# Optimization experiments

Hardware: AMD Instinct MI355X
Metric: run time of the kernel (lower is better)

## Reference

```python
import jax, jax.numpy as jnp
import numpy as np

EPS = 1e-7
PI = np.pi


def _vel_to_R(vel):
    # vel: [..., 3] -> rotation matrix [..., 3, 3] (ZY convention from spherical angles)
    rho = jnp.linalg.norm(vel, axis=-1, keepdims=True)
    theta = jnp.arctan2(vel[..., 1:2], vel[..., 0:1])
    theta = theta + (theta < 0).astype(theta.dtype) * (2.0 * PI)  # symmetric_theta=False
    phi = jnp.arccos(jnp.clip(vel[..., 2:3] / (rho + EPS), -1.0, 1.0))
    ct, st = jnp.cos(theta)[..., 0], jnp.sin(theta)[..., 0]
    cp, sp = jnp.cos(phi)[..., 0], jnp.sin(phi)[..., 0]
    z = jnp.zeros_like(ct)
    R = jnp.stack([
        jnp.stack([cp * ct, -st, sp * ct], -1),
        jnp.stack([cp * st, ct, sp * st], -1),
        jnp.stack([-sp, z, cp], -1),
    ], -2)
    return R


def _rotate(R, x):
    return jnp.einsum('...ij,...j->...i', R, x)


def setup_inputs() -> dict:
    key = jax.random.key(0)
    B, N, H, D = 128, 100, 128, 3
    in_size = 2 * D  # 6
    nef = 3 * D + D * (D - 1) // 2 + in_size  # 18 edge features
    ks = jax.random.split(key, 12)

    inputs = jax.random.normal(ks[0], (B, N, in_size), jnp.float32)

    # fully connected edges (no self loops)
    send_np, recv_np = np.nonzero(~np.eye(N, dtype=bool))
    send_edges = jnp.asarray(send_np, jnp.int32)
    recv_edges = jnp.asarray(recv_np, jnp.int32)

    def lin(k, fin, fout):
        return jax.random.normal(k, (fin, fout), jnp.float32) / np.sqrt(fin)

    return dict(
        inputs=inputs,
        W1=lin(ks[1], nef, H), b1=jnp.zeros((H,), jnp.float32),
        W2=lin(ks[2], H, H), b2=jnp.zeros((H,), jnp.float32),
        Wr=lin(ks[3], in_size, H), br=jnp.zeros((H,), jnp.float32),
        W3=lin(ks[4], H, H), b3=jnp.zeros((H,), jnp.float32),
        W4=lin(ks[5], H, H), b4=jnp.zeros((H,), jnp.float32),
        W5=lin(ks[6], H, in_size), b5=jnp.zeros((in_size,), jnp.float32),
        send_edges=send_edges, recv_edges=recv_edges,
    )


def reference(inputs, W1, b1, W2, b2, Wr, br, W3, b3, W4, b4, W5, b5,
              send_edges, recv_edges):
    D = 3
    B, N, _ = inputs.shape

    # ---- Localizer.canonicalize_inputs ----
    vel = inputs[..., D:2 * D]
    Rnode = _vel_to_R(vel)                       # [B,N,3,3]
    Rinv_node = jnp.swapaxes(Rnode, -1, -2)
    canon_vel = _rotate(Rinv_node, vel)
    rel_feat = jnp.concatenate([jnp.zeros_like(canon_vel), canon_vel], -1)  # [B,N,6]

    # ---- Localizer.create_edge_attr ----
    x_j = inputs[:, send_edges]                  # [B,E,6] senders
    x_i = inputs[:, recv_edges]                  # [B,E,6] receivers
    R = _vel_to_R(x_i[..., D:2 * D])
    R_inv = jnp.swapaxes(R, -1, -2)
    rel_pos = x_j[..., :D] - x_i[..., :D]
    rot_rel = _rotate(R_inv, rel_pos)
    send_R = _vel_to_R(x_j[..., D:2 * D])
    rot_or = R_inv @ send_R
    euler = jnp.stack([
        jnp.arctan2(rot_or[..., 1, 0], rot_or[..., 0, 0]),
        jnp.arcsin(-rot_or[..., 2, 0]),
        jnp.arctan2(rot_or[..., 2, 1], rot_or[..., 2, 2]),
    ], -1) / PI
    dist = jnp.linalg.norm(rel_pos, axis=-1, keepdims=True)
    rho_e = jnp.linalg.norm(rot_rel, axis=-1, keepdims=True)
    theta_e = jnp.arctan2(rot_rel[..., 1:2], rot_rel[..., 0:1])  # symmetric theta
    phi_e = jnp.arccos(jnp.clip(rot_rel[..., 2:3] / (rho_e + EPS), -1.0, 1.0))
    rot_vel = _rotate(R_inv, x_j[..., D:2 * D])
    edge_attr = jnp.concatenate(
        [rot_rel, euler, dist, theta_e, phi_e, rot_vel], -1)   # [B,E,12]
    edge_attr = jnp.concatenate([edge_attr, rel_feat[:, recv_edges]], -1)  # [B,E,18]

    # ---- GNN: edge MLP + scatter-mean + out MLP (dropout off in eval) ----
    h = jax.nn.silu(edge_attr @ W1 + b1) @ W2 + b2               # [B,E,H]
    agg = jnp.zeros((B, N, h.shape[-1]), h.dtype).at[:, recv_edges].add(h)
    cnt = jnp.zeros((N,), h.dtype).at[recv_edges].add(1.0)
    agg = agg / jnp.maximum(cnt, 1.0)[None, :, None]             # scatter mean
    aug = agg + rel_feat @ Wr + br
    p = jax.nn.relu(aug @ W3 + b3)
    p = jax.nn.relu(p @ W4 + b4)
    pred = p @ W5 + b5                                           # [B,N,6]

    # ---- Globalizer: rotate each 3-vector chunk back to global frame ----
    gl = jnp.concatenate(
        [_rotate(Rnode, pred[..., i:i + D]) for i in range(0, pred.shape[-1], D)], -1)
    return inputs + gl
```

## Files before the change

### kernel.cpp

```cpp
#include <hip/hip_runtime.h>
#include <math.h>

#define EPSF 1e-7f
constexpr int NN  = 100;
constexpr int DEG = 99;
constexpr int IN  = 6;
constexpr int H   = 128;
constexpr int G   = 4;
constexpr float INV_PI = 0.3183098861837907f;
constexpr float LOG2E  = 1.4426950408889634f;
constexpr float LN2    = 0.6931471805599453f;

typedef __attribute__((ext_vector_type(4))) _Float16 half4;
typedef __attribute__((ext_vector_type(8))) _Float16 half8;
typedef __attribute__((ext_vector_type(4))) float f32x4;

constexpr int XST = 144;
constexpr int SXS = 15;
constexpr int TS  = 50;
constexpr int NT  = 25;

__device__ __forceinline__ float clampf(float x, float lo, float hi) {
    return fminf(fmaxf(x, lo), hi);
}
__device__ __forceinline__ float sig2(float y) {
    return __builtin_amdgcn_rcpf(1.f + __builtin_amdgcn_exp2f(-y));
}
__device__ __forceinline__ float fast_atan2(float y, float x) {
    float ax = fabsf(x), ay = fabsf(y);
    float mx = fmaxf(ax, ay), mn = fminf(ax, ay);
    float r = mn * __builtin_amdgcn_rcpf(fmaxf(mx, 1e-35f));
    float r2 = r * r;
    float p = fmaf(r2, -0.0851330f, 0.1801410f);
    p = fmaf(r2, p, -0.3302995f);
    p = fmaf(r2, p, 0.9998660f);
    float t = r * p;
    t = (ay > ax) ? (1.5707963267948966f - t) : t;
    t = (x < 0.f) ? (3.14159265358979323f - t) : t;
    return copysignf(t, y);
}
__device__ __forceinline__ float fast_asin(float z) {
    return fast_atan2(z, sqrtf(fmaxf(0.f, (1.f - z) * (1.f + z))));
}
__device__ __forceinline__ float fast_acos(float z) {
    return fast_atan2(sqrtf(fmaxf(0.f, (1.f - z) * (1.f + z))), z);
}
__device__ __forceinline__ void vel_to_R(float vx, float vy, float vz, float* R) {
    float rho = sqrtf(vx * vx + vy * vy + vz * vz);
    float rxy = sqrtf(vx * vx + vy * vy);
    float inv = __builtin_amdgcn_rcpf(rxy);
    bool big = rxy > 1e-30f;
    float ct = big ? vx * inv : 1.f;
    float st = big ? vy * inv : 0.f;
    float cp = clampf(vz * __builtin_amdgcn_rcpf(rho + EPSF), -1.f, 1.f);
    float sp = sqrtf(fmaxf(0.f, 1.f - cp * cp));
    R[0] = cp * ct; R[1] = -st; R[2] = sp * ct;
    R[3] = cp * st; R[4] = ct;  R[5] = sp * st;
    R[6] = -sp;     R[7] = 0.f; R[8] = cp;
}

__global__ void conv_w(const float* __restrict__ W1, const float* __restrict__ W2,
                       const float* __restrict__ W3, const float* __restrict__ W4,
                       half4* __restrict__ w1f, half8* __restrict__ wmlp) {
    int t = blockIdx.x * blockDim.x + threadIdx.x;
    if (t >= 104 * 64) return;
    int L = t & 63, f = t >> 6;
    int m = L & 15, qd = L >> 4;
    if (f < 8) {
        int n = f * 16 + m;
        half4 v;
#pragma unroll
        for (int j = 0; j < 4; ++j) {
            int k = qd * 4 + j;
            v[j] = (k < 12) ? (_Float16)(W1[k * H + n] * LOG2E) : (_Float16)0.f;
        }
        w1f[f * 64 + L] = v;
    } else {
        int ff = f - 8;
        int layer = ff >> 5, rest = ff & 31;
        int kt = rest >> 3, nt = rest & 7;
        const float* W = (layer == 0) ? W2 : (layer == 1) ? W3 : W4;
        float scale = (layer == 0) ? LN2 : 1.f;
        int n = nt * 16 + m;
        half8 v;
#pragma unroll
        for (int j = 0; j < 8; ++j)
            v[j] = (_Float16)(W[(kt * 32 + qd * 8 + j) * H + n] * scale);
        wmlp[((layer * 4 + kt) * 8 + nt) * 64 + L] = v;
    }
}

__global__ __launch_bounds__(256, 8)
void locs_fused(const float* __restrict__ in,
                const float* __restrict__ W1, const float* __restrict__ b1,
                const float* __restrict__ b2,
                const float* __restrict__ Wr, const float* __restrict__ br,
                const float* __restrict__ b3, const float* __restrict__ b4,
                const float* __restrict__ W5, const float* __restrict__ b5,
                const half4* __restrict__ w1f, const half8* __restrict__ wmlp,
                float* __restrict__ out) {
    __shared__ _Float16 hpool[NT * TS * 4];
    __shared__ float sxr[NN * SXS];
    __shared__ float xFp[G * 132];
    __shared__ float cvF[16];
    __shared__ float pbF[G * 96];
    __shared__ float predF[G * 8];

    const int tid = threadIdx.x;
    const int L   = tid & 63;
    const int wv  = tid >> 6;
    const int q   = L >> 4;
    const int lm  = L & 15;
    const int bn0 = blockIdx.x * G;
    const int bB  = bn0 / NN;
    const int n0  = bn0 - bB * NN;

    {
        half4 z = {0, 0, 0, 0};
        for (int i = tid; i < NT * TS; i += 256) *(half4*)&hpool[i * 4] = z;
    }
    if (tid < NN) {
        const float* xi = in + (bB * NN + tid) * IN;
        float R[9];
        float px = xi[0], py = xi[1], pz = xi[2];
        float vx = xi[3], vy = xi[4], vz = xi[5];
        vel_to_R(vx, vy, vz, R);
        float* dst = sxr + tid * SXS;
#pragma unroll
        for (int k = 0; k < 9; ++k) dst[k] = R[k];
        dst[9] = px; dst[10] = py; dst[11] = pz;
        dst[12] = vx; dst[13] = vy; dst[14] = vz;
        int g = tid - n0;
        if ((unsigned)g < (unsigned)G) {
            cvF[g * 4 + 0] = R[0] * vx + R[3] * vy + R[6] * vz;
            cvF[g * 4 + 1] = R[1] * vx + R[4] * vy + R[7] * vz;
            cvF[g * 4 + 2] = R[2] * vx + R[5] * vy + R[8] * vz;
        }
    }
    __syncthreads();

    float bs[2];
    {
        float cv0 = cvF[q * 4 + 0], cv1 = cvF[q * 4 + 1], cv2 = cvF[q * 4 + 2];
#pragma unroll
        for (int i = 0; i < 2; ++i) {
            int ch = wv * 32 + i * 16 + lm;
            bs[i] = (b1[ch] + cv0 * W1[15 * H + ch] + cv1 * W1[16 * H + ch]
                   + cv2 * W1[17 * H + ch]) * LOG2E;
        }
    }
    half4 bfr[2];
#pragma unroll
    for (int i = 0; i < 2; ++i) bfr[i] = w1f[(wv * 2 + i) * 64 + L];

#pragma unroll
    for (int rnd = 0; rnd < 2; ++rnd) {
        int j = tid + rnd * 256;
        if (j < G * DEG) {
            int g = j / DEG;
            int e = j - g * DEG;
            int nG = n0 + g;
            int s = e < nG ? e : e + 1;
            const float* rn = sxr + nG * SXS;
            const float* rs = sxr + s * SXS;
            float Rn[9];
#pragma unroll
            for (int k = 0; k < 9; ++k) Rn[k] = rn[k];
            float rel0 = rs[9] - rn[9], rel1 = rs[10] - rn[10], rel2 = rs[11] - rn[11];
            float vjx = rs[12], vjy = rs[13], vjz = rs[14];
            float Rs0 = rs[0], Rs1 = rs[1], Rs2 = rs[2];
            float Rs3 = rs[3], Rs4 = rs[4], Rs5 = rs[5];
            float Rs6 = rs[6], Rs7 = rs[7], Rs8 = rs[8];
            float rr0 = Rn[0] * rel0 + Rn[3] * rel1 + Rn[6] * rel2;
            float rr1 = Rn[1] * rel0 + Rn[4] * rel1 + Rn[7] * rel2;
            float rr2 = Rn[2] * rel0 + Rn[5] * rel1 + Rn[8] * rel2;
            float ro00 = Rn[0] * Rs0 + Rn[3] * Rs3 + Rn[6] * Rs6;
            float ro10 = Rn[1] * Rs0 + Rn[4] * Rs3 + Rn[7] * Rs6;
            float ro20 = Rn[2] * Rs0 + Rn[5] * Rs3 + Rn[8] * Rs6;
            float ro21 = Rn[2] * Rs1 + Rn[5] * Rs4 + Rn[8] * Rs7;
            float ro22 = Rn[2] * Rs2 + Rn[5] * Rs5 + Rn[8] * Rs8;
            float dist = sqrtf(rel0 * rel0 + rel1 * rel1 + rel2 * rel2);
            half4 f0, f1, f2;
            f0[0] = (_Float16)rr0; f0[1] = (_Float16)rr1; f0[2] = (_Float16)rr2;
            f0[3] = (_Float16)(fast_atan2(ro10, ro00) * INV_PI);
            f1[0] = (_Float16)(fast_asin(clampf(-ro20, -1.f, 1.f)) * INV_PI);
            f1[1] = (_Float16)(fast_atan2(ro21, ro22) * INV_PI);
            f1[2] = (_Float16)dist;
            f1[3] = (_Float16)fast_atan2(rr1, rr0);
            f2[0] = (_Float16)fast_acos(clampf(rr2 * __builtin_amdgcn_rcpf(dist + EPSF), -1.f, 1.f));
            f2[1] = (_Float16)(Rn[0] * vjx + Rn[3] * vjy + Rn[6] * vjz);
            f2[2] = (_Float16)(Rn[1] * vjx + Rn[4] * vjy + Rn[7] * vjz);
            f2[3] = (_Float16)(Rn[2] * vjx + Rn[5] * vjy + Rn[8] * vjz);
            int t = e >> 2;
            int mrow = g * 4 + (e & 3);
            _Float16* dst = hpool + (t * TS + mrow) * 4;
            *(half4*)(dst +   0)      = f0;
            *(half4*)(dst + 16 * 4)   = f1;
            *(half4*)(dst + 32 * 4)   = f2;
        }
    }
    __syncthreads();

    {
        float part[2] = {0.f, 0.f};
        f32x4 c[2];
#pragma unroll
        for (int i = 0; i < 2; ++i) c[i] = (f32x4){bs[i], bs[i], bs[i], bs[i]};
        const int loff = (q < 3) ? (q * 16 + lm) : 48;
        half4 a_cur = *(const half4*)&hpool[(0 * TS + loff) * 4];
#pragma unroll
        for (int t = 0; t < NT; ++t) {
            half4 a_next;
            if (t < NT - 1) a_next = *(const half4*)&hpool[((t + 1) * TS + loff) * 4];
            f32x4 d0 = __builtin_amdgcn_mfma_f32_16x16x16f16(a_cur, bfr[0], c[0], 0, 0, 0);
            f32x4 d1 = __builtin_amdgcn_mfma_f32_16x16x16f16(a_cur, bfr[1], c[1], 0, 0, 0);
#pragma unroll
            for (int r = 0; r < 4; ++r) {
                part[0] += d0[r] * sig2(d0[r]);
                part[1] += d1[r] * sig2(d1[r]);
            }
            a_cur = a_next;
        }
#pragma unroll
        for (int i = 0; i < 2; ++i)
            xFp[q * 132 + wv * 32 + i * 16 + lm] = part[i] - bs[i] * sig2(bs[i]);
    }
    __syncthreads();

    _Float16* xh = hpool;
#pragma unroll
    for (int layer = 0; layer < 3; ++layer) {
        {
            int col = tid & 127, rh = tid >> 7;
#pragma unroll
            for (int r = 0; r < 2; ++r) {
                int row = r * 2 + rh;
                xh[row * XST + col] = (_Float16)xFp[row * 132 + col];
            }
        }
        half8 bh[8];
#pragma unroll
        for (int kt = 0; kt < 4; ++kt) {
            int base = ((layer * 4 + kt) * 8 + wv * 2) * 64 + L;
#pragma unroll
            for (int i = 0; i < 2; ++i) bh[kt * 2 + i] = wmlp[base + i * 64];
        }
        __syncthreads();
        int rowb = (lm & 3) * XST;
        half8 ah[4];
#pragma unroll
        for (int kt = 0; kt < 4; ++kt)
            ah[kt] = *(const half8*)&xh[rowb + kt * 32 + q * 8];
        f32x4 acc[2];
#pragma unroll
        for (int i = 0; i < 2; ++i) acc[i] = (f32x4){0.f, 0.f, 0.f, 0.f};
#pragma unroll
        for (int kt = 0; kt < 4; ++kt)
#pragma unroll
            for (int i = 0; i < 2; ++i)
                acc[i] = __builtin_amdgcn_mfma_f32_16x16x32_f16(ah[kt], bh[kt * 2 + i],
                                                                acc[i], 0, 0, 0);
        __syncthreads();
        if (L < 16) {
#pragma unroll
            for (int i = 0; i < 2; ++i) {
                int ch = (wv * 2 + i) * 16 + lm;
                if (layer == 0) {
                    float b2c = b2[ch], brc = br[ch];
                    float w3c = Wr[3 * H + ch], w4c = Wr[4 * H + ch], w5c = Wr[5 * H + ch];
#pragma unroll
                    for (int r = 0; r < 4; ++r)
                        xFp[r * 132 + ch] = acc[i][r] * (1.f / 99.f) + b2c
                                          + cvF[r * 4 + 0] * w3c + cvF[r * 4 + 1] * w4c
                                          + cvF[r * 4 + 2] * w5c + brc;
                } else {
                    float bb = (layer == 1) ? b3[ch] : b4[ch];
#pragma unroll
                    for (int r = 0; r < 4; ++r)
                        xFp[r * 132 + ch] = fmaxf(0.f, acc[i][r] + bb);
                }
            }
        }
        __syncthreads();
    }

    if (tid < 96) {
        int o = tid >> 4, sl = tid & 15, kb = sl * 8;
        float w5[8];
#pragma unroll
        for (int j = 0; j < 8; ++j) w5[j] = W5[(kb + j) * IN + o];
#pragma unroll
        for (int g = 0; g < G; ++g) {
            float s = 0.f;
#pragma unroll
            for (int j = 0; j < 8; ++j) s = fmaf(xFp[g * 132 + kb + j], w5[j], s);
            pbF[g * 96 + sl * 6 + o] = s;
        }
    }
    __syncthreads();
    if (tid < 24) {
        int g = tid / 6, o = tid - g * 6;
        float s = b5[o];
#pragma unroll
        for (int sl = 0; sl < 16; ++sl) s += pbF[g * 96 + sl * 6 + o];
        predF[g * 8 + o] = s;
    }
    __syncthreads();
    if (tid < 24) {
        int g = tid / 6, o = tid - g * 6;
        int r = (o < 3) ? o : o - 3;
        int off = (o < 3) ? 0 : 3;
        const float* Rg = sxr + (n0 + g) * SXS;
        float gl = Rg[r * 3 + 0] * predF[g * 8 + off + 0]
                 + Rg[r * 3 + 1] * predF[g * 8 + off + 1]
                 + Rg[r * 3 + 2] * predF[g * 8 + off + 2];
        int bng = bn0 + g;
        out[bng * IN + o] = Rg[9 + o] + gl;
    }
}

extern "C" void kernel_launch(void* const* d_in, const int* in_sizes, int n_in,
                              void* d_out, int out_size, void* d_ws, size_t ws_size,
                              hipStream_t stream) {
    const float* in = (const float*)d_in[0];
    const float* W1 = (const float*)d_in[1];
    const float* b1 = (const float*)d_in[2];
    const float* W2 = (const float*)d_in[3];
    const float* b2 = (const float*)d_in[4];
    const float* Wr = (const float*)d_in[5];
    const float* br = (const float*)d_in[6];
    const float* W3 = (const float*)d_in[7];
    const float* b3 = (const float*)d_in[8];
    const float* W4 = (const float*)d_in[9];
    const float* b4 = (const float*)d_in[10];
    const float* W5 = (const float*)d_in[11];
    const float* b5 = (const float*)d_in[12];
    float* out = (float*)d_out;

    half4* w1f  = (half4*)d_ws;
    half8* wmlp = (half8*)((char*)d_ws + 4096);

    const int BN = in_sizes[0] / IN;
    conv_w<<<26, 256, 0, stream>>>(W1, W2, W3, W4, w1f, wmlp);
    locs_fused<<<BN / G, 256, 0, stream>>>(in, W1, b1, b2, Wr, br, b3, b4,
                                           W5, b5, w1f, wmlp, out);
}
```

Measured before the change: 127.3 us.

## Use polynomial SiLU without reciprocal and store MLP activations directly as fp16

Replaces the sigmoid-based SiLU (exp2 plus reciprocal) in the edge aggregation loop with a form that uses exp2 of -|d| and a degree-4 polynomial, removing the rcp transcendental. The fp32 staging buffer for MLP activations is dropped. Each layer now writes fp16 straight into a dedicated shared buffer, which removes the per-layer fp32-to-fp16 conversion pass and one barrier per layer. The cost is polynomial approximation error in SiLU and fp16 rounding of the final-layer activations before W5.

```diff
diff --git a/kernel.cpp b/kernel.cpp
--- a/kernel.cpp
+++ b/kernel.cpp
@@ -20,11 +20,19 @@
 constexpr int TS  = 50;
 constexpr int NT  = 25;
 
+constexpr float PB0 = 0.99974609f;
+constexpr float PB1 = -0.98610892f;
+constexpr float PB2 = 0.87197520f;
+constexpr float PB3 = -0.54230560f;
+constexpr float PB4 = 0.15687296f;
+
 __device__ __forceinline__ float clampf(float x, float lo, float hi) {
     return fminf(fmaxf(x, lo), hi);
 }
-__device__ __forceinline__ float sig2(float y) {
-    return __builtin_amdgcn_rcpf(1.f + __builtin_amdgcn_exp2f(-y));
+__device__ __forceinline__ float silu2(float d) {
+    float u = __builtin_amdgcn_exp2f(-fabsf(d));
+    float p = fmaf(fmaf(fmaf(fmaf(PB4, u, PB3), u, PB2), u, PB1), u, PB0);
+    return fmaf(p, fabsf(d), fminf(d, 0.f));
 }
 __device__ __forceinline__ float fast_atan2(float y, float x) {
     float ax = fabsf(x), ay = fabsf(y);
@@ -101,7 +109,7 @@
                 float* __restrict__ out) {
     __shared__ _Float16 hpool[NT * TS * 4];
     __shared__ float sxr[NN * SXS];
-    __shared__ float xFp[G * 132];
+    __shared__ _Float16 xh[G * XST];
     __shared__ float cvF[16];
     __shared__ float pbF[G * 96];
     __shared__ float predF[G * 8];
@@ -216,28 +224,19 @@
             f32x4 d1 = __builtin_amdgcn_mfma_f32_16x16x16f16(a_cur, bfr[1], c[1], 0, 0, 0);
 #pragma unroll
             for (int r = 0; r < 4; ++r) {
-                part[0] += d0[r] * sig2(d0[r]);
-                part[1] += d1[r] * sig2(d1[r]);
+                part[0] += silu2(d0[r]);
+                part[1] += silu2(d1[r]);
             }
             a_cur = a_next;
         }
 #pragma unroll
         for (int i = 0; i < 2; ++i)
-            xFp[q * 132 + wv * 32 + i * 16 + lm] = part[i] - bs[i] * sig2(bs[i]);
-    }
-    __syncthreads();
-
-    _Float16* xh = hpool;
+            xh[q * XST + wv * 32 + i * 16 + lm] = (_Float16)(part[i] - silu2(bs[i]));
+    }
+    __syncthreads();
+
 #pragma unroll
     for (int layer = 0; layer < 3; ++layer) {
-        {
-            int col = tid & 127, rh = tid >> 7;
-#pragma unroll
-            for (int r = 0; r < 2; ++r) {
-                int row = r * 2 + rh;
-                xh[row * XST + col] = (_Float16)xFp[row * 132 + col];
-            }
-        }
         half8 bh[8];
 #pragma unroll
         for (int kt = 0; kt < 4; ++kt) {
@@ -245,7 +244,6 @@
 #pragma unroll
             for (int i = 0; i < 2; ++i) bh[kt * 2 + i] = wmlp[base + i * 64];
         }
-        __syncthreads();
         int rowb = (lm & 3) * XST;
         half8 ah[4];
 #pragma unroll
@@ -270,14 +268,14 @@
                     float w3c = Wr[3 * H + ch], w4c = Wr[4 * H + ch], w5c = Wr[5 * H + ch];
 #pragma unroll
                     for (int r = 0; r < 4; ++r)
-                        xFp[r * 132 + ch] = acc[i][r] * (1.f / 99.f) + b2c
+                        xh[r * XST + ch] = (_Float16)(acc[i][r] * (1.f / 99.f) + b2c
                                           + cvF[r * 4 + 0] * w3c + cvF[r * 4 + 1] * w4c
-                                          + cvF[r * 4 + 2] * w5c + brc;
+                                          + cvF[r * 4 + 2] * w5c + brc);
                 } else {
                     float bb = (layer == 1) ? b3[ch] : b4[ch];
 #pragma unroll
                     for (int r = 0; r < 4; ++r)
-                        xFp[r * 132 + ch] = fmaxf(0.f, acc[i][r] + bb);
+                        xh[r * XST + ch] = (_Float16)fmaxf(0.f, acc[i][r] + bb);
                 }
             }
         }
@@ -291,9 +289,10 @@
         for (int j = 0; j < 8; ++j) w5[j] = W5[(kb + j) * IN + o];
 #pragma unroll
         for (int g = 0; g < G; ++g) {
+            half8 xv = *(const half8*)&xh[g * XST + kb];
             float s = 0.f;
 #pragma unroll
-            for (int j = 0; j < 8; ++j) s = fmaf(xFp[g * 132 + kb + j], w5[j], s);
+            for (int j = 0; j < 8; ++j) s = fmaf((float)xv[j], w5[j], s);
             pbF[g * 96 + sl * 6 + o] = s;
         }
     }
```

Result: slower. 142.4 us (+11.8%).

## Process two node groups per block to reuse per-batch rotation setup

Applied to the files above, without the earlier changes.

Each block now loops over two consecutive groups of four nodes, halving the grid. The per-batch node rotation table in shared memory is built once and recomputed only when the second group starts a new batch element. This amortizes the vel_to_R prologue and the weight-fragment loads across twice the work. The trade-off is fewer blocks and serialized per-block work, plus extra barriers and re-zeroing of padded rows.

```diff
diff --git a/kernel.cpp b/kernel.cpp
--- a/kernel.cpp
+++ b/kernel.cpp
@@ -111,211 +111,226 @@
     const int wv  = tid >> 6;
     const int q   = L >> 4;
     const int lm  = L & 15;
-    const int bn0 = blockIdx.x * G;
-    const int bB  = bn0 / NN;
-    const int n0  = bn0 - bB * NN;
-
-    {
-        half4 z = {0, 0, 0, 0};
-        for (int i = tid; i < NT * TS; i += 256) *(half4*)&hpool[i * 4] = z;
-    }
-    if (tid < NN) {
-        const float* xi = in + (bB * NN + tid) * IN;
-        float R[9];
-        float px = xi[0], py = xi[1], pz = xi[2];
-        float vx = xi[3], vy = xi[4], vz = xi[5];
-        vel_to_R(vx, vy, vz, R);
-        float* dst = sxr + tid * SXS;
-#pragma unroll
-        for (int k = 0; k < 9; ++k) dst[k] = R[k];
-        dst[9] = px; dst[10] = py; dst[11] = pz;
-        dst[12] = vx; dst[13] = vy; dst[14] = vz;
-        int g = tid - n0;
-        if ((unsigned)g < (unsigned)G) {
-            cvF[g * 4 + 0] = R[0] * vx + R[3] * vy + R[6] * vz;
-            cvF[g * 4 + 1] = R[1] * vx + R[4] * vy + R[7] * vz;
-            cvF[g * 4 + 2] = R[2] * vx + R[5] * vy + R[8] * vz;
-        }
-    }
-    __syncthreads();
-
-    float bs[2];
-    {
-        float cv0 = cvF[q * 4 + 0], cv1 = cvF[q * 4 + 1], cv2 = cvF[q * 4 + 2];
-#pragma unroll
-        for (int i = 0; i < 2; ++i) {
-            int ch = wv * 32 + i * 16 + lm;
-            bs[i] = (b1[ch] + cv0 * W1[15 * H + ch] + cv1 * W1[16 * H + ch]
-                   + cv2 * W1[17 * H + ch]) * LOG2E;
-        }
-    }
+
     half4 bfr[2];
 #pragma unroll
     for (int i = 0; i < 2; ++i) bfr[i] = w1f[(wv * 2 + i) * 64 + L];
 
-#pragma unroll
+#pragma unroll 1
     for (int rnd = 0; rnd < 2; ++rnd) {
-        int j = tid + rnd * 256;
-        if (j < G * DEG) {
-            int g = j / DEG;
-            int e = j - g * DEG;
-            int nG = n0 + g;
-            int s = e < nG ? e : e + 1;
-            const float* rn = sxr + nG * SXS;
-            const float* rs = sxr + s * SXS;
-            float Rn[9];
-#pragma unroll
-            for (int k = 0; k < 9; ++k) Rn[k] = rn[k];
-            float rel0 = rs[9] - rn[9], rel1 = rs[10] - rn[10], rel2 = rs[11] - rn[11];
-            float vjx = rs[12], vjy = rs[13], vjz = rs[14];
-            float Rs0 = rs[0], Rs1 = rs[1], Rs2 = rs[2];
-            float Rs3 = rs[3], Rs4 = rs[4], Rs5 = rs[5];
-            float Rs6 = rs[6], Rs7 = rs[7], Rs8 = rs[8];
-            float rr0 = Rn[0] * rel0 + Rn[3] * rel1 + Rn[6] * rel2;
-            float rr1 = Rn[1] * rel0 + Rn[4] * rel1 + Rn[7] * rel2;
-            float rr2 = Rn[2] * rel0 + Rn[5] * rel1 + Rn[8] * rel2;
-            float ro00 = Rn[0] * Rs0 + Rn[3] * Rs3 + Rn[6] * Rs6;
-            float ro10 = Rn[1] * Rs0 + Rn[4] * Rs3 + Rn[7] * Rs6;
-            float ro20 = Rn[2] * Rs0 + Rn[5] * Rs3 + Rn[8] * Rs6;
-            float ro21 = Rn[2] * Rs1 + Rn[5] * Rs4 + Rn[8] * Rs7;
-            float ro22 = Rn[2] * Rs2 + Rn[5] * Rs5 + Rn[8] * Rs8;
-            float dist = sqrtf(rel0 * rel0 + rel1 * rel1 + rel2 * rel2);
-            half4 f0, f1, f2;
-            f0[0] = (_Float16)rr0; f0[1] = (_Float16)rr1; f0[2] = (_Float16)rr2;
-            f0[3] = (_Float16)(fast_atan2(ro10, ro00) * INV_PI);
-            f1[0] = (_Float16)(fast_asin(clampf(-ro20, -1.f, 1.f)) * INV_PI);
-            f1[1] = (_Float16)(fast_atan2(ro21, ro22) * INV_PI);
-            f1[2] = (_Float16)dist;
-            f1[3] = (_Float16)fast_atan2(rr1, rr0);
-            f2[0] = (_Float16)fast_acos(clampf(rr2 * __builtin_amdgcn_rcpf(dist + EPSF), -1.f, 1.f));
-            f2[1] = (_Float16)(Rn[0] * vjx + Rn[3] * vjy + Rn[6] * vjz);
-            f2[2] = (_Float16)(Rn[1] * vjx + Rn[4] * vjy + Rn[7] * vjz);
-            f2[3] = (_Float16)(Rn[2] * vjx + Rn[5] * vjy + Rn[8] * vjz);
-            int t = e >> 2;
-            int mrow = g * 4 + (e & 3);
-            _Float16* dst = hpool + (t * TS + mrow) * 4;
-            *(half4*)(dst +   0)      = f0;
-            *(half4*)(dst + 16 * 4)   = f1;
-            *(half4*)(dst + 32 * 4)   = f2;
-        }
-    }
-    __syncthreads();
-
-    {
-        float part[2] = {0.f, 0.f};
-        f32x4 c[2];
-#pragma unroll
-        for (int i = 0; i < 2; ++i) c[i] = (f32x4){bs[i], bs[i], bs[i], bs[i]};
-        const int loff = (q < 3) ? (q * 16 + lm) : 48;
-        half4 a_cur = *(const half4*)&hpool[(0 * TS + loff) * 4];
-#pragma unroll
-        for (int t = 0; t < NT; ++t) {
-            half4 a_next;
-            if (t < NT - 1) a_next = *(const half4*)&hpool[((t + 1) * TS + loff) * 4];
-            f32x4 d0 = __builtin_amdgcn_mfma_f32_16x16x16f16(a_cur, bfr[0], c[0], 0, 0, 0);
-            f32x4 d1 = __builtin_amdgcn_mfma_f32_16x16x16f16(a_cur, bfr[1], c[1], 0, 0, 0);
-#pragma unroll
-            for (int r = 0; r < 4; ++r) {
-                part[0] += d0[r] * sig2(d0[r]);
-                part[1] += d1[r] * sig2(d1[r]);
-            }
-            a_cur = a_next;
-        }
-#pragma unroll
-        for (int i = 0; i < 2; ++i)
-            xFp[q * 132 + wv * 32 + i * 16 + lm] = part[i] - bs[i] * sig2(bs[i]);
-    }
-    __syncthreads();
-
-    _Float16* xh = hpool;
-#pragma unroll
-    for (int layer = 0; layer < 3; ++layer) {
+        const int bn0 = (blockIdx.x * 2 + rnd) * G;
+        const int bB  = bn0 / NN;
+        const int n0  = bn0 - bB * NN;
+
+        if (rnd == 0) {
+            half4 z = {0, 0, 0, 0};
+            for (int i = tid; i < NT * TS; i += 256) *(half4*)&hpool[i * 4] = z;
+        }
+        if (rnd == 0 || n0 == 0) {
+            if (tid < NN) {
+                const float* xi = in + (bB * NN + tid) * IN;
+                float R[9];
+                float px = xi[0], py = xi[1], pz = xi[2];
+                float vx = xi[3], vy = xi[4], vz = xi[5];
+                vel_to_R(vx, vy, vz, R);
+                float* dst = sxr + tid * SXS;
+#pragma unroll
+                for (int k = 0; k < 9; ++k) dst[k] = R[k];
+                dst[9] = px; dst[10] = py; dst[11] = pz;
+                dst[12] = vx; dst[13] = vy; dst[14] = vz;
+            }
+        }
+        __syncthreads();
+        if (tid < G) {
+            const float* rg = sxr + (n0 + tid) * SXS;
+            float vx = rg[12], vy = rg[13], vz = rg[14];
+            cvF[tid * 4 + 0] = rg[0] * vx + rg[3] * vy + rg[6] * vz;
+            cvF[tid * 4 + 1] = rg[1] * vx + rg[4] * vy + rg[7] * vz;
+            cvF[tid * 4 + 2] = rg[2] * vx + rg[5] * vy + rg[8] * vz;
+        }
+        __syncthreads();
+
+        float bs[2];
         {
-            int col = tid & 127, rh = tid >> 7;
-#pragma unroll
-            for (int r = 0; r < 2; ++r) {
-                int row = r * 2 + rh;
-                xh[row * XST + col] = (_Float16)xFp[row * 132 + col];
-            }
-        }
-        half8 bh[8];
-#pragma unroll
-        for (int kt = 0; kt < 4; ++kt) {
-            int base = ((layer * 4 + kt) * 8 + wv * 2) * 64 + L;
-#pragma unroll
-            for (int i = 0; i < 2; ++i) bh[kt * 2 + i] = wmlp[base + i * 64];
-        }
-        __syncthreads();
-        int rowb = (lm & 3) * XST;
-        half8 ah[4];
-#pragma unroll
-        for (int kt = 0; kt < 4; ++kt)
-            ah[kt] = *(const half8*)&xh[rowb + kt * 32 + q * 8];
-        f32x4 acc[2];
-#pragma unroll
-        for (int i = 0; i < 2; ++i) acc[i] = (f32x4){0.f, 0.f, 0.f, 0.f};
-#pragma unroll
-        for (int kt = 0; kt < 4; ++kt)
+            float cv0 = cvF[q * 4 + 0], cv1 = cvF[q * 4 + 1], cv2 = cvF[q * 4 + 2];
+#pragma unroll
+            for (int i = 0; i < 2; ++i) {
+                int ch = wv * 32 + i * 16 + lm;
+                bs[i] = (b1[ch] + cv0 * W1[15 * H + ch] + cv1 * W1[16 * H + ch]
+                       + cv2 * W1[17 * H + ch]) * LOG2E;
+            }
+        }
+
+        if (rnd && tid < NT) {
+            half4 z = {0, 0, 0, 0};
+            *(half4*)&hpool[(tid * TS + 48) * 4] = z;
+        }
+
+#pragma unroll
+        for (int rr = 0; rr < 2; ++rr) {
+            int j = tid + rr * 256;
+            if (j < G * DEG) {
+                int g = j / DEG;
+                int e = j - g * DEG;
+                int nG = n0 + g;
+                int s = e < nG ? e : e + 1;
+                const float* rn = sxr + nG * SXS;
+                const float* rs = sxr + s * SXS;
+                float Rn[9];
+#pragma unroll
+                for (int k = 0; k < 9; ++k) Rn[k] = rn[k];
+                float rel0 = rs[9] - rn[9], rel1 = rs[10] - rn[10], rel2 = rs[11] - rn[11];
+                float vjx = rs[12], vjy = rs[13], vjz = rs[14];
+                float Rs0 = rs[0], Rs1 = rs[1], Rs2 = rs[2];
+                float Rs3 = rs[3], Rs4 = rs[4], Rs5 = rs[5];
+                float Rs6 = rs[6], Rs7 = rs[7], Rs8 = rs[8];
+                float rr0 = Rn[0] * rel0 + Rn[3] * rel1 + Rn[6] * rel2;
+                float rr1 = Rn[1] * rel0 + Rn[4] * rel1 + Rn[7] * rel2;
+                float rr2 = Rn[2] * rel0 + Rn[5] * rel1 + Rn[8] * rel2;
+                float ro00 = Rn[0] * Rs0 + Rn[3] * Rs3 + Rn[6] * Rs6;
+                float ro10 = Rn[1] * Rs0 + Rn[4] * Rs3 + Rn[7] * Rs6;
+                float ro20 = Rn[2] * Rs0 + Rn[5] * Rs3 + Rn[8] * Rs6;
+                float ro21 = Rn[2] * Rs1 + Rn[5] * Rs4 + Rn[8] * Rs7;
+                float ro22 = Rn[2] * Rs2 + Rn[5] * Rs5 + Rn[8] * Rs8;
+                float dist = sqrtf(rel0 * rel0 + rel1 * rel1 + rel2 * rel2);
+                half4 f0, f1, f2;
+                f0[0] = (_Float16)rr0; f0[1] = (_Float16)rr1; f0[2] = (_Float16)rr2;
+                f0[3] = (_Float16)(fast_atan2(ro10, ro00) * INV_PI);
+                f1[0] = (_Float16)(fast_asin(clampf(-ro20, -1.f, 1.f)) * INV_PI);
+                f1[1] = (_Float16)(fast_atan2(ro21, ro22) * INV_PI);
+                f1[2] = (_Float16)dist;
+                f1[3] = (_Float16)fast_atan2(rr1, rr0);
+                f2[0] = (_Float16)fast_acos(clampf(rr2 * __builtin_amdgcn_rcpf(dist + EPSF), -1.f, 1.f));
+                f2[1] = (_Float16)(Rn[0] * vjx + Rn[3] * vjy + Rn[6] * vjz);
+                f2[2] = (_Float16)(Rn[1] * vjx + Rn[4] * vjy + Rn[7] * vjz);
+                f2[3] = (_Float16)(Rn[2] * vjx + Rn[5] * vjy + Rn[8] * vjz);
+                int t = e >> 2;
+                int mrow = g * 4 + (e & 3);
+                _Float16* dst = hpool + (t * TS + mrow) * 4;
+                *(half4*)(dst +   0)      = f0;
+                *(half4*)(dst + 16 * 4)   = f1;
+                *(half4*)(dst + 32 * 4)   = f2;
+            }
+        }
+        __syncthreads();
+
+        {
+            float part[2] = {0.f, 0.f};
+            f32x4 c[2];
+#pragma unroll
+            for (int i = 0; i < 2; ++i) c[i] = (f32x4){bs[i], bs[i], bs[i], bs[i]};
+            const int loff = (q < 3) ? (q * 16 + lm) : 48;
+            half4 a_cur = *(const half4*)&hpool[(0 * TS + loff) * 4];
+#pragma unroll
+            for (int t = 0; t < NT; ++t) {
+                half4 a_next;
+                if (t < NT - 1) a_next = *(const half4*)&hpool[((t + 1) * TS + loff) * 4];
+                f32x4 d0 = __builtin_amdgcn_mfma_f32_16x16x16f16(a_cur, bfr[0], c[0], 0, 0, 0);
+                f32x4 d1 = __builtin_amdgcn_mfma_f32_16x16x16f16(a_cur, bfr[1], c[1], 0, 0, 0);
+#pragma unroll
+                for (int r = 0; r < 4; ++r) {
+                    part[0] += d0[r] * sig2(d0[r]);
+                    part[1] += d1[r] * sig2(d1[r]);
+                }
+                a_cur = a_next;
+            }
 #pragma unroll
             for (int i = 0; i < 2; ++i)
-                acc[i] = __builtin_amdgcn_mfma_f32_16x16x32_f16(ah[kt], bh[kt * 2 + i],
-                                                                acc[i], 0, 0, 0);
-        __syncthreads();
-        if (L < 16) {
-#pragma unroll
-            for (int i = 0; i < 2; ++i) {
-                int ch = (wv * 2 + i) * 16 + lm;
-                if (layer == 0) {
-                    float b2c = b2[ch], brc = br[ch];
-                    float w3c = Wr[3 * H + ch], w4c = Wr[4 * H + ch], w5c = Wr[5 * H + ch];
-#pragma unroll
-                    for (int r = 0; r < 4; ++r)
-                        xFp[r * 132 + ch] = acc[i][r] * (1.f / 99.f) + b2c
-                                          + cvF[r * 4 + 0] * w3c + cvF[r * 4 + 1] * w4c
-                                          + cvF[r * 4 + 2] * w5c + brc;
-                } else {
-                    float bb = (layer == 1) ? b3[ch] : b4[ch];
-#pragma unroll
-                    for (int r = 0; r < 4; ++r)
-                        xFp[r * 132 + ch] = fmaxf(0.f, acc[i][r] + bb);
+                xFp[q * 132 + wv * 32 + i * 16 + lm] = part[i] - bs[i] * sig2(bs[i]);
+        }
+        __syncthreads();
+
+        _Float16* xh = hpool;
+#pragma unroll
+        for (int layer = 0; layer < 3; ++layer) {
+            {
+                int col = tid & 127, rh = tid >> 7;
+#pragma unroll
+                for (int r = 0; r < 2; ++r) {
+                    int row = r * 2 + rh;
+                    xh[row * XST + col] = (_Float16)xFp[row * 132 + col];
                 }
             }
-        }
-        __syncthreads();
-    }
-
-    if (tid < 96) {
-        int o = tid >> 4, sl = tid & 15, kb = sl * 8;
-        float w5[8];
-#pragma unroll
-        for (int j = 0; j < 8; ++j) w5[j] = W5[(kb + j) * IN + o];
-#pragma unroll
-        for (int g = 0; g < G; ++g) {
-            float s = 0.f;
-#pragma unroll
-            for (int j = 0; j < 8; ++j) s = fmaf(xFp[g * 132 + kb + j], w5[j], s);
-            pbF[g * 96 + sl * 6 + o] = s;
-        }
-    }
-    __syncthreads();
-    if (tid < 24) {
-        int g = tid / 6, o = tid - g * 6;
-        float s = b5[o];
-#pragma unroll
-        for (int sl = 0; sl < 16; ++sl) s += pbF[g * 96 + sl * 6 + o];
-        predF[g * 8 + o] = s;
-    }
-    __syncthreads();
-    if (tid < 24) {
-        int g = tid / 6, o = tid - g * 6;
-        int r = (o < 3) ? o : o - 3;
-        int off = (o < 3) ? 0 : 3;
-        const float* Rg = sxr + (n0 + g) * SXS;
-        float gl = Rg[r * 3 + 0] * predF[g * 8 + off + 0]
-                 + Rg[r * 3 + 1] * predF[g * 8 + off + 1]
-                 + Rg[r * 3 + 2] * predF[g * 8 + off + 2];
-        int bng = bn0 + g;
-        out[bng * IN + o] = Rg[9 + o] + gl;
+            half8 bh[8];
+#pragma unroll
+            for (int kt = 0; kt < 4; ++kt) {
+                int base = ((layer * 4 + kt) * 8 + wv * 2) * 64 + L;
+#pragma unroll
+                for (int i = 0; i < 2; ++i) bh[kt * 2 + i] = wmlp[base + i * 64];
+            }
+            __syncthreads();
+            int rowb = (lm & 3) * XST;
+            half8 ah[4];
+#pragma unroll
+            for (int kt = 0; kt < 4; ++kt)
+                ah[kt] = *(const half8*)&xh[rowb + kt * 32 + q * 8];
+            f32x4 acc[2];
+#pragma unroll
+            for (int i = 0; i < 2; ++i) acc[i] = (f32x4){0.f, 0.f, 0.f, 0.f};
+#pragma unroll
+            for (int kt = 0; kt < 4; ++kt)
+#pragma unroll
+                for (int i = 0; i < 2; ++i)
+                    acc[i] = __builtin_amdgcn_mfma_f32_16x16x32_f16(ah[kt], bh[kt * 2 + i],
+                                                                    acc[i], 0, 0, 0);
+            __syncthreads();
+            if (L < 16) {
+#pragma unroll
+                for (int i = 0; i < 2; ++i) {
+                    int ch = (wv * 2 + i) * 16 + lm;
+                    if (layer == 0) {
+                        float b2c = b2[ch], brc = br[ch];
+                        float w3c = Wr[3 * H + ch], w4c = Wr[4 * H + ch], w5c = Wr[5 * H + ch];
+#pragma unroll
+                        for (int r = 0; r < 4; ++r)
+                            xFp[r * 132 + ch] = acc[i][r] * (1.f / 99.f) + b2c
+                                              + cvF[r * 4 + 0] * w3c + cvF[r * 4 + 1] * w4c
+                                              + cvF[r * 4 + 2] * w5c + brc;
+                    } else {
+                        float bb = (layer == 1) ? b3[ch] : b4[ch];
+#pragma unroll
+                        for (int r = 0; r < 4; ++r)
+                            xFp[r * 132 + ch] = fmaxf(0.f, acc[i][r] + bb);
+                    }
+                }
+            }
+            __syncthreads();
+        }
+
+        if (tid < 96) {
+            int o = tid >> 4, sl = tid & 15, kb = sl * 8;
+            float w5[8];
+#pragma unroll
+            for (int j = 0; j < 8; ++j) w5[j] = W5[(kb + j) * IN + o];
+#pragma unroll
+            for (int g = 0; g < G; ++g) {
+                float s = 0.f;
+#pragma unroll
+                for (int j = 0; j < 8; ++j) s = fmaf(xFp[g * 132 + kb + j], w5[j], s);
+                pbF[g * 96 + sl * 6 + o] = s;
+            }
+        }
+        __syncthreads();
+        if (tid < 24) {
+            int g = tid / 6, o = tid - g * 6;
+            float s = b5[o];
+#pragma unroll
+            for (int sl = 0; sl < 16; ++sl) s += pbF[g * 96 + sl * 6 + o];
+            predF[g * 8 + o] = s;
+        }
+        __syncthreads();
+        if (tid < 24) {
+            int g = tid / 6, o = tid - g * 6;
+            int r = (o < 3) ? o : o - 3;
+            int off = (o < 3) ? 0 : 3;
+            const float* Rg = sxr + (n0 + g) * SXS;
+            float gl = Rg[r * 3 + 0] * predF[g * 8 + off + 0]
+                     + Rg[r * 3 + 1] * predF[g * 8 + off + 1]
+                     + Rg[r * 3 + 2] * predF[g * 8 + off + 2];
+            int bng = bn0 + g;
+            out[bng * IN + o] = Rg[9 + o] + gl;
+        }
+        __syncthreads();
     }
 }
 
@@ -342,6 +357,6 @@
 
     const int BN = in_sizes[0] / IN;
     conv_w<<<26, 256, 0, stream>>>(W1, W2, W3, W4, w1f, wmlp);
-    locs_fused<<<BN / G, 256, 0, stream>>>(in, W1, b1, b2, Wr, br, b3, b4,
-                                           W5, b5, w1f, wmlp, out);
-}
+    locs_fused<<<BN / (2 * G), 256, 0, stream>>>(in, W1, b1, b2, Wr, br, b3, b4,
+                                                 W5, b5, w1f, wmlp, out);
+}
```

Measured after the change: 179.3 us. +40.8%, slower.
